# Kernel optimization log

Measured on AMD Instinct MI355X. Metric: run time of the kernel, lower is better.

## Reference

```python
import jax, jax.numpy as jnp
import numpy as np

EPS = 1e-5
GN_GROUPS_DIV = 4  # nn.GroupNorm(out_ch // 4, out_ch)


def conv1x1(x, w, b=None):
    # x [B,C,H,W], w [O,C]
    y = jnp.einsum('bchw,oc->bohw', x, w)
    return y if b is None else y + b[None, :, None, None]


def conv2d(x, w, pad):
    return jax.lax.conv_general_dilated(
        x, w, (1, 1), [(pad, pad), (pad, pad)],
        dimension_numbers=('NCHW', 'OIHW', 'NCHW'))


def batchnorm(x, gamma, beta):
    # training-mode BatchNorm2d: batch statistics over (B,H,W)
    mu = jnp.mean(x, axis=(0, 2, 3), keepdims=True)
    var = jnp.var(x, axis=(0, 2, 3), keepdims=True)
    xn = (x - mu) * jax.lax.rsqrt(var + EPS)
    return xn * gamma[None, :, None, None] + beta[None, :, None, None]


def groupnorm(x, gamma, beta, groups):
    B, C, H, W = x.shape
    xg = x.reshape(B, groups, C // groups, H, W)
    mu = jnp.mean(xg, axis=(2, 3, 4), keepdims=True)
    var = jnp.var(xg, axis=(2, 3, 4), keepdims=True)
    xn = ((xg - mu) * jax.lax.rsqrt(var + EPS)).reshape(B, C, H, W)
    return xn * gamma[None, :, None, None] + beta[None, :, None, None]


def bilinear_sample(img, ys, xs):
    # Faithful to DSC._bilinear_interpolate_3D: floor/floor+1 coords are
    # clamped BEFORE computing weights, so samples exactly at the last
    # row/col get all-zero weights (output zeroed there), as in torch.
    H, W = img.shape[2], img.shape[3]
    y0 = jnp.floor(ys)
    x0 = jnp.floor(xs)
    y0c = jnp.clip(y0, 0, H - 1).astype(jnp.int32)
    y1c = jnp.clip(y0 + 1, 0, H - 1).astype(jnp.int32)
    x0c = jnp.clip(x0, 0, W - 1).astype(jnp.int32)
    x1c = jnp.clip(x0 + 1, 0, W - 1).astype(jnp.int32)
    y0f, y1f = y0c.astype(ys.dtype), y1c.astype(ys.dtype)
    x0f, x1f = x0c.astype(xs.dtype), x1c.astype(xs.dtype)
    w00 = (y1f - ys) * (x1f - xs)
    w01 = (y1f - ys) * (xs - x0f)
    w10 = (ys - y0f) * (x1f - xs)
    w11 = (ys - y0f) * (xs - x0f)
    g = lambda yy, xx: img[:, :, yy, xx]  # irregular gather, [B,C,H,W]
    return (g(y0c, x0c) * w00 + g(y0c, x1c) * w01 +
            g(y1c, x0c) * w10 + g(y1c, x1c) * w11)


def _forward(x, ca_w1, ca_w2, sa_w, gate_w, off_w, off_b, off_gamma, off_beta,
             dsc_w, dsc_b, gn_gamma, gn_beta, bn_gamma, bn_beta, prelu_a,
             out_w, out_b):
    B, C, H, W = x.shape
    res = x

    # --- ChannelAttention2D (CBAM): shared MLP on avg & max pooled desc ---
    avg = jnp.mean(x, axis=(2, 3), keepdims=True)          # [B,C,1,1]
    mx = jnp.max(x, axis=(2, 3), keepdims=True)
    mlp = lambda v: conv1x1(jax.nn.relu(conv1x1(v, ca_w1)), ca_w2)
    ca = jax.nn.sigmoid(mlp(avg) + mlp(mx))
    x_ca = x * ca

    # --- SpatialAttention2D (CBAM): 7x7 conv over [mean,max] channel maps ---
    s_avg = jnp.mean(x, axis=1, keepdims=True)
    s_max = jnp.max(x, axis=1, keepdims=True)
    sa = jax.nn.sigmoid(conv2d(jnp.concatenate([s_avg, s_max], axis=1), sa_w, pad=3))
    x_sa = x * sa

    # --- gate fuse ---
    fuse = x_sa + x_ca
    guide = jax.nn.sigmoid(conv1x1(fuse, gate_w))
    xg = x * guide

    # --- DSConv(kernel_size=1, morph=0, if_offset=True) ---
    # offset branch (computed as in torch; with num_points=1 the iterative
    # offset accumulation zeroes the center point, so offsets do NOT move
    # the sampling grid -> zero gradient flows to the offset conv)
    off = jnp.tanh(batchnorm(conv2d(xg, off_w, pad=1) + off_b[None, :, None, None],
                             off_gamma, off_beta))
    del off  # dead in fwd math for kernel_size=1 (faithful to source)

    ii = jnp.arange(H, dtype=x.dtype)[:, None] * jnp.ones((1, W), x.dtype)
    jj = jnp.ones((H, 1), x.dtype) * jnp.arange(W, dtype=x.dtype)[None, :]
    deformed = bilinear_sample(xg, ii, jj)  # identity gather except last row/col zeroed

    d = conv1x1(deformed, dsc_w, dsc_b)     # dsc_conv_x with (k,1)=(1,1) kernel
    d = groupnorm(d, gn_gamma, gn_beta, C // GN_GROUPS_DIV)
    d = jax.nn.relu(d)

    # --- residual + BN + PReLU + 1x1 out conv ---
    y = d + res
    y = batchnorm(y, bn_gamma, bn_beta)
    a = prelu_a.reshape(())
    y = jnp.where(y >= 0, y, a * y)
    return conv1x1(y, out_w, out_b)         # [B,1,H,W]


def setup_inputs() -> dict:
    key = jax.random.key(0)
    ks = jax.random.split(key, 12)
    B, C, H, W = 8, 64, 256, 256
    r = C // 16  # CBAM ratio 16
    f32 = jnp.float32
    n = lambda k, shp, s: (jax.random.normal(k, shp, dtype=f32) * s)
    return {
        'x': n(ks[0], (B, C, H, W), 1.0),
        'ca_w1': n(ks[1], (r, C), 0.1),
        'ca_w2': n(ks[2], (C, r), 0.1),
        'sa_w': n(ks[3], (1, 2, 7, 7), 0.1),
        'gate_w': n(ks[4], (C, C), 0.05),
        'off_w': n(ks[5], (2, C, 3, 3), 0.05),
        'off_b': jnp.zeros((2,), f32),
        'off_gamma': jnp.ones((2,), f32),
        'off_beta': jnp.zeros((2,), f32),
        'dsc_w': n(ks[6], (C, C), 0.05),
        'dsc_b': jnp.zeros((C,), f32),
        'gn_gamma': jnp.ones((C,), f32),
        'gn_beta': jnp.zeros((C,), f32),
        'bn_gamma': jnp.ones((C,), f32),
        'bn_beta': jnp.zeros((C,), f32),
        'prelu_a': jnp.full((1,), 0.25, f32),
        'out_w': n(ks[7], (1, C), 0.1),
        'out_b': jnp.zeros((1,), f32),
    }


def reference(x, ca_w1, ca_w2, sa_w, gate_w, off_w, off_b, off_gamma, off_beta,
              dsc_w, dsc_b, gn_gamma, gn_beta, bn_gamma, bn_beta, prelu_a,
              out_w, out_b):
    return _forward(x, ca_w1, ca_w2, sa_w, gate_w, off_w, off_b, off_gamma,
                    off_beta, dsc_w, dsc_b, gn_gamma, gn_beta, bn_gamma,
                    bn_beta, prelu_a, out_w, out_b)
```

## Files before the change

### kernel.cpp

```cpp
#include <hip/hip_runtime.h>

#define HW 65536
#define CB 64
#define NB 8

typedef __attribute__((ext_vector_type(4))) float f32x4;
typedef __attribute__((ext_vector_type(8))) short s16x8;

__device__ __forceinline__ float sigm(float v) { return 1.f / (1.f + __expf(-v)); }

__device__ __forceinline__ unsigned encf(float f) {
    unsigned u = __float_as_uint(f);
    return (u & 0x80000000u) ? ~u : (u | 0x80000000u);
}
__device__ __forceinline__ float decf(unsigned u) {
    return (u & 0x80000000u) ? __uint_as_float(u & 0x7fffffffu) : __uint_as_float(~u);
}
__device__ __forceinline__ unsigned f2bf(float f) {
    unsigned u = __float_as_uint(f);
    u += 0x7fffu + ((u >> 16) & 1u);
    return u >> 16;
}
__device__ __forceinline__ float bf2f(unsigned h) {
    return __uint_as_float(h << 16);
}
__device__ __forceinline__ int swz(int row, int w) { return (row << 5) + (w ^ ((row & 7) << 2)); }

__global__ __launch_bounds__(256) void k_init(
    const float* __restrict__ gw, const float* __restrict__ dw,
    unsigned* __restrict__ wbuf, unsigned* __restrict__ stats)
{
    const int t = threadIdx.x;
    if (blockIdx.x < 2) {
        const float* src = (blockIdx.x == 0) ? gw : dw;
        unsigned* dst = wbuf + (blockIdx.x << 11);
        const int orow = t >> 2, cq = (t & 3) << 4;
        const float* s = src + (orow << 6) + cq;
        unsigned u[8];
        #pragma unroll
        for (int j = 0; j < 8; ++j)
            u[j] = f2bf(s[2 * j]) | (f2bf(s[2 * j + 1]) << 16);
        const int wbase = (t & 3) << 3;
        *(uint4*)&dst[swz(orow, wbase)]     = make_uint4(u[0], u[1], u[2], u[3]);
        *(uint4*)&dst[swz(orow, wbase + 4)] = make_uint4(u[4], u[5], u[6], u[7]);
    } else {
        const int base = (blockIdx.x - 2) * 4736;
        #pragma unroll
        for (int k = 0; k < 19; ++k) {
            const int idx = base + k * 256 + t;
            if (idx < base + 4736 && idx < 9472) stats[idx] = 0u;
        }
    }
}

__global__ __launch_bounds__(256) void k_pre(
    const float* __restrict__ x, unsigned short* __restrict__ xpc,
    float* __restrict__ pool_scr, unsigned* __restrict__ pmax_scr,
    unsigned* __restrict__ sm)
{
    __shared__ unsigned tile[8192];
    __shared__ float scrS[8][64];
    __shared__ float scrM[8][64];
    const int t = threadIdx.x;
    const int b = blockIdx.x >> 8;
    const int pbase = (blockIdx.x & 255) << 8;
    const size_t xb = ((size_t)(b << 6)) * HW + pbase + t;
    const int s = (t & 7) << 2;

    float psum = 0.f, pmax = -1e30f;
    #pragma unroll
    for (int cg = 0; cg < 4; ++cg) {
        float v[16];
        #pragma unroll
        for (int k = 0; k < 16; ++k)
            v[k] = x[xb + (size_t)((cg << 4) + k) * HW];
        #pragma unroll
        for (int k = 0; k < 16; ++k) { psum += v[k]; pmax = fmaxf(pmax, v[k]); }
        unsigned w[8];
        #pragma unroll
        for (int k = 0; k < 8; ++k) w[k] = f2bf(v[2 * k]) | (f2bf(v[2 * k + 1]) << 16);
        *(uint4*)&tile[(t << 5) + (((cg << 3)) ^ s)]     = make_uint4(w[0], w[1], w[2], w[3]);
        *(uint4*)&tile[(t << 5) + (((cg << 3) + 4) ^ s)] = make_uint4(w[4], w[5], w[6], w[7]);
    }
    sm[(size_t)b * HW + pbase + t] = f2bf(psum * (1.f / 64.f)) | (f2bf(pmax) << 16);
    __syncthreads();

    {
        const int cp = t & 31, q = t >> 5;
        float s0 = 0.f, s1 = 0.f, m0 = -1e30f, m1 = -1e30f;
        #pragma unroll 8
        for (int i = 0; i < 32; ++i) {
            const int px = (q << 5) + i;
            const unsigned u = tile[(px << 5) + (cp ^ ((px & 7) << 2))];
            const float a0 = bf2f(u & 0xffffu), a1 = bf2f(u >> 16);
            s0 += a0; s1 += a1;
            m0 = fmaxf(m0, a0); m1 = fmaxf(m1, a1);
        }
        scrS[q][2 * cp] = s0; scrS[q][2 * cp + 1] = s1;
        scrM[q][2 * cp] = m0; scrM[q][2 * cp + 1] = m1;
    }
    {
        unsigned short* xp = xpc + (((size_t)b * HW + pbase) << 6);
        #pragma unroll
        for (int k = 0; k < 8; ++k) {
            const int px = (k << 5) + (t >> 3);
            const int w = ((t & 7) << 2) ^ ((px & 7) << 2);
            const uint4 v = *(const uint4*)&tile[(px << 5) + w];
            *(uint4*)(xp + (k << 11) + (t << 3)) = v;
        }
    }
    __syncthreads();
    if (t < 64) {
        float ss = 0.f, mm = -1e30f;
        #pragma unroll
        for (int q = 0; q < 8; ++q) { ss += scrS[q][t]; mm = fmaxf(mm, scrM[q][t]); }
        const int copy = blockIdx.x & 7;
        atomicAdd(&pool_scr[(((b << 3) + copy) << 6) + t], ss);
        atomicMax(&pmax_scr[(((b << 3) + copy) << 6) + t], encf(mm));
    }
}

__global__ __launch_bounds__(256) void k_sa_ca(
    const unsigned* __restrict__ sm, const float* __restrict__ w,
    const float* __restrict__ pool_scr, const unsigned* __restrict__ pmax_scr,
    const float* __restrict__ w1, const float* __restrict__ w2,
    unsigned short* __restrict__ sa, float* __restrict__ ca)
{
    const int t = threadIdx.x;
    const int b = blockIdx.x >> 8;
    const int pix = ((blockIdx.x & 255) << 8) | t;
    const int i = pix >> 8, j = pix & 255;
    const unsigned* src = sm + (size_t)b * HW;
    float acc = 0.f;
    #pragma unroll
    for (int ki = 0; ki < 7; ++ki) {
        const int y = i + ki - 3;
        if ((unsigned)y < 256u) {
            #pragma unroll
            for (int kj = 0; kj < 7; ++kj) {
                const int xx = j + kj - 3;
                if ((unsigned)xx < 256u) {
                    const unsigned u = src[(y << 8) | xx];
                    acc += bf2f(u & 0xffffu) * w[ki * 7 + kj] +
                           bf2f(u >> 16)     * w[49 + ki * 7 + kj];
                }
            }
        }
    }
    sa[(size_t)b * HW + pix] = (unsigned short)f2bf(sigm(acc));

    if ((blockIdx.x & 255) == 0) {
        __shared__ float av[CB], mv[CB], hh[8];
        if (t < CB) {
            float ss = 0.f; unsigned mm = 0u;
            #pragma unroll
            for (int r = 0; r < 8; ++r) {
                ss += pool_scr[(((b << 3) + r) << 6) + t];
                mm = max(mm, pmax_scr[(((b << 3) + r) << 6) + t]);
            }
            av[t] = ss * (1.f / (float)HW);
            mv[t] = decf(mm);
        }
        __syncthreads();
        if (t < 8) {
            const int h = t & 3;
            const float* v = (t < 4) ? av : mv;
            float ssum = 0;
            for (int c = 0; c < CB; ++c) ssum += w1[h * CB + c] * v[c];
            hh[t] = fmaxf(ssum, 0.f);
        }
        __syncthreads();
        if (t < CB) {
            float ssum = 0;
            #pragma unroll
            for (int h = 0; h < 4; ++h) ssum += w2[t * 4 + h] * (hh[h] + hh[4 + h]);
            ca[b * CB + t] = sigm(ssum);
        }
    }
}

__global__ __launch_bounds__(256, 3) void k_main(
    const unsigned short* __restrict__ xpc, const unsigned short* __restrict__ sa,
    const float* __restrict__ ca, const unsigned* __restrict__ wbuf,
    const float* __restrict__ db,
    unsigned short* __restrict__ dbuf, float* __restrict__ gn_sum,
    float* __restrict__ gn_sq)
{
    __shared__ unsigned lds[12320];
    __shared__ float saL[128];
    __shared__ float caL[64];
    const int t = threadIdx.x;
    const int wv = t >> 6, l = t & 63, hi = l >> 4, lo = l & 15;
    const int b = blockIdx.x >> 9;
    const int pbase = (blockIdx.x & 511) << 7;

    #pragma unroll
    for (int k = 0; k < 4; ++k) {
        const int idx = (k << 8) + t;
        *(uint4*)&lds[idx << 2] = *(const uint4*)&wbuf[idx << 2];
    }
    if (t < 128) saL[t] = bf2f(sa[(size_t)b * HW + pbase + t]);
    else if (t < 192) caL[t - 128] = ca[(b << 6) + (t - 128)];

    {
        const unsigned short* xp = xpc + (((size_t)b * HW + pbase) << 6);
        #pragma unroll
        for (int k = 0; k < 4; ++k) {
            const int idx = (k << 8) + t;
            const int px = idx >> 3;
            const int wg = (idx & 7) << 2;
            const uint4 v = *(const uint4*)(xp + (idx << 3));
            *(uint4*)&lds[8192 + (px << 5) + (wg ^ ((px & 7) << 2))] = v;
        }
    }
    __syncthreads();

    {
        const int wb2 = (wv << 3) + (hi << 1);
        const int cbb = wb2 << 1;
        const float c0 = caL[cbb], c1 = caL[cbb + 1], c2 = caL[cbb + 2], c3 = caL[cbb + 3];
        #pragma unroll
        for (int n = 0; n < 8; ++n) {
            const int pxl = (n << 4) + lo;
            const float sv = saL[pxl];
            const uint2 xv = *(const uint2*)&lds[8192 + swz(pxl, wb2)];
            uint2 o;
            o.x = f2bf(bf2f(xv.x & 0xffffu) * (sv + c0)) | (f2bf(bf2f(xv.x >> 16) * (sv + c1)) << 16);
            o.y = f2bf(bf2f(xv.y & 0xffffu) * (sv + c2)) | (f2bf(bf2f(xv.y >> 16) * (sv + c3)) << 16);
            *(uint2*)&lds[4096 + swz(pxl, wb2)] = o;
        }
    }
    __syncthreads();

    f32x4 acc[8];
    #pragma unroll
    for (int n = 0; n < 8; ++n) acc[n] = (f32x4){0.f, 0.f, 0.f, 0.f};
    {
        const int arow = (wv << 4) + lo;
        const s16x8 a0 = __builtin_bit_cast(s16x8, *(const uint4*)&lds[swz(arow, hi << 2)]);
        const s16x8 a1 = __builtin_bit_cast(s16x8, *(const uint4*)&lds[swz(arow, (hi << 2) + 16)]);
        #pragma unroll
        for (int n = 0; n < 8; ++n) {
            const int brow = (n << 4) + lo;
            const s16x8 b0 = __builtin_bit_cast(s16x8, *(const uint4*)&lds[4096 + swz(brow, hi << 2)]);
            const s16x8 b1 = __builtin_bit_cast(s16x8, *(const uint4*)&lds[4096 + swz(brow, (hi << 2) + 16)]);
            acc[n] = __builtin_amdgcn_mfma_f32_16x16x32_bf16(a0, b0, acc[n], 0, 0, 0);
            acc[n] = __builtin_amdgcn_mfma_f32_16x16x32_bf16(a1, b1, acc[n], 0, 0, 0);
        }
    }
    __syncthreads();

    {
        const bool row255 = (pbase >> 8) == 255;
        const bool halfblk = (pbase & 128) != 0;
        const int wb2 = (wv << 3) + (hi << 1);
        #pragma unroll
        for (int n = 0; n < 8; ++n) {
            const int pxl = (n << 4) + lo;
            const uint2 xv = *(const uint2*)&lds[8192 + swz(pxl, wb2)];
            const bool zero = row255 || (halfblk && pxl == 127);
            float xg0 = zero ? 0.f : bf2f(xv.x & 0xffffu) * sigm(acc[n][0]);
            float xg1 = zero ? 0.f : bf2f(xv.x >> 16)     * sigm(acc[n][1]);
            float xg2 = zero ? 0.f : bf2f(xv.y & 0xffffu) * sigm(acc[n][2]);
            float xg3 = zero ? 0.f : bf2f(xv.y >> 16)     * sigm(acc[n][3]);
            uint2 o;
            o.x = f2bf(xg0) | (f2bf(xg1) << 16);
            o.y = f2bf(xg2) | (f2bf(xg3) << 16);
            *(uint2*)&lds[4096 + swz(pxl, wb2)] = o;
        }
    }
    __syncthreads();

    f32x4 acc2[8];
    #pragma unroll
    for (int n = 0; n < 8; ++n) acc2[n] = (f32x4){0.f, 0.f, 0.f, 0.f};
    {
        const int arow = (wv << 4) + lo;
        const s16x8 a0 = __builtin_bit_cast(s16x8, *(const uint4*)&lds[2048 + swz(arow, hi << 2)]);
        const s16x8 a1 = __builtin_bit_cast(s16x8, *(const uint4*)&lds[2048 + swz(arow, (hi << 2) + 16)]);
        #pragma unroll
        for (int n = 0; n < 8; ++n) {
            const int brow = (n << 4) + lo;
            const s16x8 b0 = __builtin_bit_cast(s16x8, *(const uint4*)&lds[4096 + swz(brow, hi << 2)]);
            const s16x8 b1 = __builtin_bit_cast(s16x8, *(const uint4*)&lds[4096 + swz(brow, (hi << 2) + 16)]);
            acc2[n] = __builtin_amdgcn_mfma_f32_16x16x32_bf16(a0, b0, acc2[n], 0, 0, 0);
            acc2[n] = __builtin_amdgcn_mfma_f32_16x16x32_bf16(a1, b1, acc2[n], 0, 0, 0);
        }
    }

    float gs = 0.f, gq = 0.f;
    {
        const float4 bv = *(const float4*)(db + (wv << 4) + (hi << 2));
        unsigned short* dp = dbuf + (((size_t)b * HW + pbase) << 6) + (wv << 4) + (hi << 2);
        #pragma unroll
        for (int n = 0; n < 8; ++n) {
            const int pxl = (n << 4) + lo;
            const float d0 = acc2[n][0] + bv.x, d1 = acc2[n][1] + bv.y;
            const float d2 = acc2[n][2] + bv.z, d3 = acc2[n][3] + bv.w;
            gs += d0 + d1 + d2 + d3;
            gq += d0 * d0 + d1 * d1 + d2 * d2 + d3 * d3;
            uint2 o;
            o.x = f2bf(d0) | (f2bf(d1) << 16);
            o.y = f2bf(d2) | (f2bf(d3) << 16);
            *(uint2*)(dp + ((size_t)pxl << 6)) = o;
        }
    }
    #pragma unroll
    for (int o = 1; o < 16; o <<= 1) { gs += __shfl_xor(gs, o); gq += __shfl_xor(gq, o); }
    float* smf = (float*)&lds[12288];
    if (lo == 0) { smf[(((wv << 2) + hi) << 1)] = gs; smf[(((wv << 2) + hi) << 1) + 1] = gq; }
    __syncthreads();
    if (t < 16) {
        atomicAdd(&gn_sum[(b << 4) + t], smf[2 * t]);
        atomicAdd(&gn_sq[(b << 4) + t],  smf[2 * t + 1]);
    }
}

__global__ __launch_bounds__(256) void k_gnbn(
    const unsigned short* __restrict__ xpc, unsigned short* __restrict__ dy,
    const float* __restrict__ gn_sum, const float* __restrict__ gn_sq,
    const float* __restrict__ gamma, const float* __restrict__ beta,
    float* __restrict__ bn_scr)
{
    const int t = threadIdx.x;
    const size_t P0 = (size_t)blockIdx.x << 8;
    const int b = (int)(P0 >> 16);
    __shared__ float ga[CB], gb[CB];
    __shared__ float red[4][128];
    if (t < CB) {
        const int g = t >> 2;
        const float n4 = 4.f * (float)HW;
        const float mu = gn_sum[b * 16 + g] / n4;
        const float var = gn_sq[b * 16 + g] / n4 - mu * mu;
        const float a = rsqrtf(var + 1e-5f) * gamma[t];
        ga[t] = a; gb[t] = beta[t] - mu * a;
    }
    __syncthreads();
    const int o8 = (t & 7) << 3;
    float ar[8], br[8];
    #pragma unroll
    for (int k = 0; k < 8; ++k) { ar[k] = ga[o8 + k]; br[k] = gb[o8 + k]; }
    float as[8], aq[8];
    #pragma unroll
    for (int k = 0; k < 8; ++k) { as[k] = 0.f; aq[k] = 0.f; }
    for (int i = 0; i < 8; ++i) {
        const size_t P = P0 + (i << 5) + (t >> 3);
        const size_t idx = (P << 6) + o8;
        const uint4 dv = *(const uint4*)(dy + idx);
        const uint4 xv = *(const uint4*)(xpc + idx);
        const unsigned dw_[4] = {dv.x, dv.y, dv.z, dv.w};
        const unsigned xw_[4] = {xv.x, xv.y, xv.z, xv.w};
        uint4 o;
        unsigned ow_[4];
        #pragma unroll
        for (int p = 0; p < 4; ++p) {
            const int k0 = 2 * p;
            const float y0 = fmaxf(bf2f(dw_[p] & 0xffffu) * ar[k0] + br[k0], 0.f) + bf2f(xw_[p] & 0xffffu);
            const float y1 = fmaxf(bf2f(dw_[p] >> 16) * ar[k0 + 1] + br[k0 + 1], 0.f) + bf2f(xw_[p] >> 16);
            as[k0] += y0; aq[k0] += y0 * y0;
            as[k0 + 1] += y1; aq[k0 + 1] += y1 * y1;
            ow_[p] = f2bf(y0) | (f2bf(y1) << 16);
        }
        o.x = ow_[0]; o.y = ow_[1]; o.z = ow_[2]; o.w = ow_[3];
        *(uint4*)(dy + idx) = o;
    }
    #pragma unroll
    for (int k = 0; k < 8; ++k) {
        #pragma unroll
        for (int m = 8; m < 64; m <<= 1) {
            as[k] += __shfl_xor(as[k], m);
            aq[k] += __shfl_xor(aq[k], m);
        }
    }
    if ((t & 63) < 8) {
        const int o = t & 7, wvv = t >> 6;
        #pragma unroll
        for (int k = 0; k < 8; ++k) {
            red[wvv][o * 16 + k] = as[k];
            red[wvv][o * 16 + 8 + k] = aq[k];
        }
    }
    __syncthreads();
    if (t < 128) {
        const int o = t >> 4, st = (t >> 3) & 1, k = t & 7;
        const float v = red[0][t] + red[1][t] + red[2][t] + red[3][t];
        atomicAdd(&bn_scr[(blockIdx.x & 7) * 128 + st * 64 + o * 8 + k], v);
    }
}

__global__ __launch_bounds__(256) void k_out(
    const unsigned short* __restrict__ y, const float* __restrict__ bn_scr,
    const float* __restrict__ gamma, const float* __restrict__ beta,
    const float* __restrict__ pa, const float* __restrict__ ow,
    const float* __restrict__ ob, float* __restrict__ out)
{
    const int t = threadIdx.x;
    __shared__ float A[CB], Bs[CB], W[CB];
    if (t < CB) {
        float s = 0.f, q = 0.f;
        #pragma unroll
        for (int r = 0; r < 8; ++r) { s += bn_scr[r * 128 + t]; q += bn_scr[r * 128 + 64 + t]; }
        const float n = (float)NB * (float)HW;
        const float mu = s / n;
        const float var = q / n - mu * mu;
        const float a = rsqrtf(var + 1e-5f) * gamma[t];
        A[t] = a; Bs[t] = beta[t] - mu * a; W[t] = ow[t];
    }
    __syncthreads();
    const size_t P = ((size_t)blockIdx.x << 8) + t;
    const unsigned short* yp = y + (P << 6);
    const float alpha = pa[0];
    float acc = ob[0];
    #pragma unroll
    for (int q = 0; q < 8; ++q) {
        const uint4 v = *(const uint4*)(yp + (q << 3));
        const unsigned vw[4] = {v.x, v.y, v.z, v.w};
        #pragma unroll
        for (int p = 0; p < 4; ++p) {
            const int c = (q << 3) + 2 * p;
            float z0 = bf2f(vw[p] & 0xffffu) * A[c] + Bs[c];
            float z1 = bf2f(vw[p] >> 16) * A[c + 1] + Bs[c + 1];
            z0 = z0 >= 0.f ? z0 : alpha * z0;
            z1 = z1 >= 0.f ? z1 : alpha * z1;
            acc += W[c] * z0 + W[c + 1] * z1;
        }
    }
    out[P] = acc;
}

extern "C" void kernel_launch(void* const* d_in, const int* in_sizes, int n_in,
                              void* d_out, int out_size, void* d_ws, size_t ws_size,
                              hipStream_t stream)
{
    const float* x        = (const float*)d_in[0];
    const float* ca_w1    = (const float*)d_in[1];
    const float* ca_w2    = (const float*)d_in[2];
    const float* sa_w     = (const float*)d_in[3];
    const float* gate_w   = (const float*)d_in[4];
    const float* dsc_w    = (const float*)d_in[9];
    const float* dsc_b    = (const float*)d_in[10];
    const float* gn_gamma = (const float*)d_in[11];
    const float* gn_beta  = (const float*)d_in[12];
    const float* bn_gamma = (const float*)d_in[13];
    const float* bn_beta  = (const float*)d_in[14];
    const float* prelu_a  = (const float*)d_in[15];
    const float* out_w    = (const float*)d_in[16];
    const float* out_b    = (const float*)d_in[17];
    float* out = (float*)d_out;

    char* ws = (char*)d_ws;
    size_t off = 0;
    auto alloc = [&](size_t bytes) -> char* {
        char* p = ws + off;
        off = (off + bytes + 255) & ~(size_t)255;
        return p;
    };
    unsigned short* dbuf = (unsigned short*)alloc((size_t)NB * HW * CB * 2);
    unsigned short* xpc  = (unsigned short*)alloc((size_t)NB * HW * CB * 2);
    unsigned* smb        = (unsigned*)alloc((size_t)NB * HW * 4);
    unsigned short* sab  = (unsigned short*)alloc((size_t)NB * HW * 2);
    unsigned* wbuf       = (unsigned*)alloc(4096 * 4);
    float* cav   = (float*)alloc(512 * 4);
    char* stats  = alloc(9472 * 4);
    float*    pool_scr = (float*)stats;
    unsigned* pmax_scr = (unsigned*)(stats + 4096 * 4);
    float*    gn_sum   = (float*)(stats + 8192 * 4);
    float*    gn_sq    = (float*)(stats + 8320 * 4);
    float*    bn_scr   = (float*)(stats + 8448 * 4);
    (void)in_sizes; (void)n_in; (void)out_size; (void)ws_size;

    k_init <<<4,        256, 0, stream>>>(gate_w, dsc_w, wbuf, (unsigned*)stats);
    k_pre  <<<NB * 256, 256, 0, stream>>>(x, xpc, pool_scr, pmax_scr, smb);
    k_sa_ca<<<NB * 256, 256, 0, stream>>>(smb, sa_w, pool_scr, pmax_scr,
                                          ca_w1, ca_w2, sab, cav);
    k_main <<<NB * 512, 256, 0, stream>>>(xpc, sab, cav, wbuf, dsc_b,
                                          dbuf, gn_sum, gn_sq);
    k_gnbn <<<2048,     256, 0, stream>>>(xpc, dbuf, gn_sum, gn_sq, gn_gamma, gn_beta, bn_scr);
    k_out  <<<2048,     256, 0, stream>>>(dbuf, bn_scr, bn_gamma, bn_beta,
                                          prelu_a, out_w, out_b, out);
}
```

Baseline: 164.6 us.

## Fold init into k_pre, drop pooling atomics, load weights to registers in k_main

Removes the separate k_init launch by adding three extra blocks to k_pre that convert the weights and zero the stats. Channel pooling partials are now written per block without atomics and reduced over 256 entries in k_sa_ca. In k_main the gate and dsc weight fragments are read straight from global memory into registers, and the attention scaling is fused into the LDS fill stage. This shrinks LDS use so occupancy can be raised to 4 blocks. The costs are a serial 256-step reduction in one block per batch and register pressure at the higher occupancy.

```diff
diff --git a/kernel.cpp b/kernel.cpp
--- a/kernel.cpp
+++ b/kernel.cpp
@@ -9,13 +9,6 @@
 
 __device__ __forceinline__ float sigm(float v) { return 1.f / (1.f + __expf(-v)); }
 
-__device__ __forceinline__ unsigned encf(float f) {
-    unsigned u = __float_as_uint(f);
-    return (u & 0x80000000u) ? ~u : (u | 0x80000000u);
-}
-__device__ __forceinline__ float decf(unsigned u) {
-    return (u & 0x80000000u) ? __uint_as_float(u & 0x7fffffffu) : __uint_as_float(~u);
-}
 __device__ __forceinline__ unsigned f2bf(float f) {
     unsigned u = __float_as_uint(f);
     u += 0x7fffu + ((u >> 16) & 1u);
@@ -26,42 +19,38 @@
 }
 __device__ __forceinline__ int swz(int row, int w) { return (row << 5) + (w ^ ((row & 7) << 2)); }
 
-__global__ __launch_bounds__(256) void k_init(
-    const float* __restrict__ gw, const float* __restrict__ dw,
-    unsigned* __restrict__ wbuf, unsigned* __restrict__ stats)
-{
-    const int t = threadIdx.x;
-    if (blockIdx.x < 2) {
-        const float* src = (blockIdx.x == 0) ? gw : dw;
-        unsigned* dst = wbuf + (blockIdx.x << 11);
-        const int orow = t >> 2, cq = (t & 3) << 4;
-        const float* s = src + (orow << 6) + cq;
-        unsigned u[8];
-        #pragma unroll
-        for (int j = 0; j < 8; ++j)
-            u[j] = f2bf(s[2 * j]) | (f2bf(s[2 * j + 1]) << 16);
-        const int wbase = (t & 3) << 3;
-        *(uint4*)&dst[swz(orow, wbase)]     = make_uint4(u[0], u[1], u[2], u[3]);
-        *(uint4*)&dst[swz(orow, wbase + 4)] = make_uint4(u[4], u[5], u[6], u[7]);
-    } else {
-        const int base = (blockIdx.x - 2) * 4736;
-        #pragma unroll
-        for (int k = 0; k < 19; ++k) {
-            const int idx = base + k * 256 + t;
-            if (idx < base + 4736 && idx < 9472) stats[idx] = 0u;
-        }
-    }
-}
-
 __global__ __launch_bounds__(256) void k_pre(
     const float* __restrict__ x, unsigned short* __restrict__ xpc,
-    float* __restrict__ pool_scr, unsigned* __restrict__ pmax_scr,
-    unsigned* __restrict__ sm)
-{
+    float* __restrict__ pool_scr, float* __restrict__ pmax_scr,
+    unsigned* __restrict__ sm,
+    const float* __restrict__ gw, const float* __restrict__ dw,
+    unsigned* __restrict__ wbuf, float* __restrict__ zstats)
+{
+    const int t = threadIdx.x;
+    if (blockIdx.x >= NB * 256) {
+        const int ex = blockIdx.x - NB * 256;
+        if (ex < 2) {
+            const float* src = (ex == 0) ? gw : dw;
+            unsigned* dst = wbuf + (ex << 11);
+            const int orow = t >> 2, cq = (t & 3) << 4;
+            const float* s = src + (orow << 6) + cq;
+            unsigned u[8];
+            #pragma unroll
+            for (int j = 0; j < 8; ++j)
+                u[j] = f2bf(s[2 * j]) | (f2bf(s[2 * j + 1]) << 16);
+            const int wbase = (t & 3) << 3;
+            *(uint4*)&dst[swz(orow, wbase)]     = make_uint4(u[0], u[1], u[2], u[3]);
+            *(uint4*)&dst[swz(orow, wbase + 4)] = make_uint4(u[4], u[5], u[6], u[7]);
+        } else {
+            #pragma unroll
+            for (int k2 = 0; k2 < 5; ++k2) zstats[k2 * 256 + t] = 0.f;
+        }
+        return;
+    }
+
     __shared__ unsigned tile[8192];
     __shared__ float scrS[8][64];
     __shared__ float scrM[8][64];
-    const int t = threadIdx.x;
     const int b = blockIdx.x >> 8;
     const int pbase = (blockIdx.x & 255) << 8;
     const size_t xb = ((size_t)(b << 6)) * HW + pbase + t;
@@ -114,15 +103,14 @@
         float ss = 0.f, mm = -1e30f;
         #pragma unroll
         for (int q = 0; q < 8; ++q) { ss += scrS[q][t]; mm = fmaxf(mm, scrM[q][t]); }
-        const int copy = blockIdx.x & 7;
-        atomicAdd(&pool_scr[(((b << 3) + copy) << 6) + t], ss);
-        atomicMax(&pmax_scr[(((b << 3) + copy) << 6) + t], encf(mm));
+        pool_scr[((size_t)blockIdx.x << 6) + t] = ss;
+        pmax_scr[((size_t)blockIdx.x << 6) + t] = mm;
     }
 }
 
 __global__ __launch_bounds__(256) void k_sa_ca(
     const unsigned* __restrict__ sm, const float* __restrict__ w,
-    const float* __restrict__ pool_scr, const unsigned* __restrict__ pmax_scr,
+    const float* __restrict__ pool_scr, const float* __restrict__ pmax_scr,
     const float* __restrict__ w1, const float* __restrict__ w2,
     unsigned short* __restrict__ sa, float* __restrict__ ca)
 {
@@ -152,14 +140,13 @@
     if ((blockIdx.x & 255) == 0) {
         __shared__ float av[CB], mv[CB], hh[8];
         if (t < CB) {
-            float ss = 0.f; unsigned mm = 0u;
-            #pragma unroll
-            for (int r = 0; r < 8; ++r) {
-                ss += pool_scr[(((b << 3) + r) << 6) + t];
-                mm = max(mm, pmax_scr[(((b << 3) + r) << 6) + t]);
+            float ss = 0.f, mm = -1e30f;
+            for (int r = 0; r < 256; ++r) {
+                ss += pool_scr[(((size_t)(b << 8) + r) << 6) + t];
+                mm = fmaxf(mm, pmax_scr[(((size_t)(b << 8) + r) << 6) + t]);
             }
             av[t] = ss * (1.f / (float)HW);
-            mv[t] = decf(mm);
+            mv[t] = mm;
         }
         __syncthreads();
         if (t < 8) {
@@ -179,28 +166,24 @@
     }
 }
 
-__global__ __launch_bounds__(256, 3) void k_main(
+__global__ __launch_bounds__(256, 4) void k_main(
     const unsigned short* __restrict__ xpc, const unsigned short* __restrict__ sa,
     const float* __restrict__ ca, const unsigned* __restrict__ wbuf,
     const float* __restrict__ db,
     unsigned short* __restrict__ dbuf, float* __restrict__ gn_sum,
     float* __restrict__ gn_sq)
 {
-    __shared__ unsigned lds[12320];
-    __shared__ float saL[128];
-    __shared__ float caL[64];
+    __shared__ unsigned lds[8224];
     const int t = threadIdx.x;
     const int wv = t >> 6, l = t & 63, hi = l >> 4, lo = l & 15;
     const int b = blockIdx.x >> 9;
     const int pbase = (blockIdx.x & 511) << 7;
 
-    #pragma unroll
-    for (int k = 0; k < 4; ++k) {
-        const int idx = (k << 8) + t;
-        *(uint4*)&lds[idx << 2] = *(const uint4*)&wbuf[idx << 2];
-    }
-    if (t < 128) saL[t] = bf2f(sa[(size_t)b * HW + pbase + t]);
-    else if (t < 192) caL[t - 128] = ca[(b << 6) + (t - 128)];
+    const int arow = (wv << 4) + lo;
+    const s16x8 ag0 = __builtin_bit_cast(s16x8, *(const uint4*)&wbuf[swz(arow, hi << 2)]);
+    const s16x8 ag1 = __builtin_bit_cast(s16x8, *(const uint4*)&wbuf[swz(arow, (hi << 2) + 16)]);
+    const s16x8 ad0 = __builtin_bit_cast(s16x8, *(const uint4*)&wbuf[2048 + swz(arow, hi << 2)]);
+    const s16x8 ad1 = __builtin_bit_cast(s16x8, *(const uint4*)&wbuf[2048 + swz(arow, (hi << 2) + 16)]);
 
     {
         const unsigned short* xp = xpc + (((size_t)b * HW + pbase) << 6);
@@ -208,26 +191,24 @@
         for (int k = 0; k < 4; ++k) {
             const int idx = (k << 8) + t;
             const int px = idx >> 3;
+            const int ch0 = (idx & 7) << 3;
             const int wg = (idx & 7) << 2;
             const uint4 v = *(const uint4*)(xp + (idx << 3));
-            *(uint4*)&lds[8192 + (px << 5) + (wg ^ ((px & 7) << 2))] = v;
-        }
-    }
-    __syncthreads();
-
-    {
-        const int wb2 = (wv << 3) + (hi << 1);
-        const int cbb = wb2 << 1;
-        const float c0 = caL[cbb], c1 = caL[cbb + 1], c2 = caL[cbb + 2], c3 = caL[cbb + 3];
-        #pragma unroll
-        for (int n = 0; n < 8; ++n) {
-            const int pxl = (n << 4) + lo;
-            const float sv = saL[pxl];
-            const uint2 xv = *(const uint2*)&lds[8192 + swz(pxl, wb2)];
-            uint2 o;
-            o.x = f2bf(bf2f(xv.x & 0xffffu) * (sv + c0)) | (f2bf(bf2f(xv.x >> 16) * (sv + c1)) << 16);
-            o.y = f2bf(bf2f(xv.y & 0xffffu) * (sv + c2)) | (f2bf(bf2f(xv.y >> 16) * (sv + c3)) << 16);
-            *(uint2*)&lds[4096 + swz(pxl, wb2)] = o;
+            const float sv = bf2f(sa[(size_t)b * HW + pbase + px]);
+            const float4 cv0 = *(const float4*)(ca + (b << 6) + ch0);
+            const float4 cv1 = *(const float4*)(ca + (b << 6) + ch0 + 4);
+            uint4 fv;
+            fv.x = f2bf(bf2f(v.x & 0xffffu) * (sv + cv0.x)) |
+                   (f2bf(bf2f(v.x >> 16)    * (sv + cv0.y)) << 16);
+            fv.y = f2bf(bf2f(v.y & 0xffffu) * (sv + cv0.z)) |
+                   (f2bf(bf2f(v.y >> 16)    * (sv + cv0.w)) << 16);
+            fv.z = f2bf(bf2f(v.z & 0xffffu) * (sv + cv1.x)) |
+                   (f2bf(bf2f(v.z >> 16)    * (sv + cv1.y)) << 16);
+            fv.w = f2bf(bf2f(v.w & 0xffffu) * (sv + cv1.z)) |
+                   (f2bf(bf2f(v.w >> 16)    * (sv + cv1.w)) << 16);
+            const int off = (px << 5) + (wg ^ ((px & 7) << 2));
+            *(uint4*)&lds[4096 + off] = v;
+            *(uint4*)&lds[off]        = fv;
         }
     }
     __syncthreads();
@@ -235,18 +216,13 @@
     f32x4 acc[8];
     #pragma unroll
     for (int n = 0; n < 8; ++n) acc[n] = (f32x4){0.f, 0.f, 0.f, 0.f};
-    {
-        const int arow = (wv << 4) + lo;
-        const s16x8 a0 = __builtin_bit_cast(s16x8, *(const uint4*)&lds[swz(arow, hi << 2)]);
-        const s16x8 a1 = __builtin_bit_cast(s16x8, *(const uint4*)&lds[swz(arow, (hi << 2) + 16)]);
-        #pragma unroll
-        for (int n = 0; n < 8; ++n) {
-            const int brow = (n << 4) + lo;
-            const s16x8 b0 = __builtin_bit_cast(s16x8, *(const uint4*)&lds[4096 + swz(brow, hi << 2)]);
-            const s16x8 b1 = __builtin_bit_cast(s16x8, *(const uint4*)&lds[4096 + swz(brow, (hi << 2) + 16)]);
-            acc[n] = __builtin_amdgcn_mfma_f32_16x16x32_bf16(a0, b0, acc[n], 0, 0, 0);
-            acc[n] = __builtin_amdgcn_mfma_f32_16x16x32_bf16(a1, b1, acc[n], 0, 0, 0);
-        }
+    #pragma unroll
+    for (int n = 0; n < 8; ++n) {
+        const int brow = (n << 4) + lo;
+        const s16x8 b0 = __builtin_bit_cast(s16x8, *(const uint4*)&lds[swz(brow, hi << 2)]);
+        const s16x8 b1 = __builtin_bit_cast(s16x8, *(const uint4*)&lds[swz(brow, (hi << 2) + 16)]);
+        acc[n] = __builtin_amdgcn_mfma_f32_16x16x32_bf16(ag0, b0, acc[n], 0, 0, 0);
+        acc[n] = __builtin_amdgcn_mfma_f32_16x16x32_bf16(ag1, b1, acc[n], 0, 0, 0);
     }
     __syncthreads();
 
@@ -257,7 +233,7 @@
         #pragma unroll
         for (int n = 0; n < 8; ++n) {
             const int pxl = (n << 4) + lo;
-            const uint2 xv = *(const uint2*)&lds[8192 + swz(pxl, wb2)];
+            const uint2 xv = *(const uint2*)&lds[4096 + swz(pxl, wb2)];
             const bool zero = row255 || (halfblk && pxl == 127);
             float xg0 = zero ? 0.f : bf2f(xv.x & 0xffffu) * sigm(acc[n][0]);
             float xg1 = zero ? 0.f : bf2f(xv.x >> 16)     * sigm(acc[n][1]);
@@ -266,7 +242,7 @@
             uint2 o;
             o.x = f2bf(xg0) | (f2bf(xg1) << 16);
             o.y = f2bf(xg2) | (f2bf(xg3) << 16);
-            *(uint2*)&lds[4096 + swz(pxl, wb2)] = o;
+            *(uint2*)&lds[swz(pxl, wb2)] = o;
         }
     }
     __syncthreads();
@@ -274,18 +250,13 @@
     f32x4 acc2[8];
     #pragma unroll
     for (int n = 0; n < 8; ++n) acc2[n] = (f32x4){0.f, 0.f, 0.f, 0.f};
-    {
-        const int arow = (wv << 4) + lo;
-        const s16x8 a0 = __builtin_bit_cast(s16x8, *(const uint4*)&lds[2048 + swz(arow, hi << 2)]);
-        const s16x8 a1 = __builtin_bit_cast(s16x8, *(const uint4*)&lds[2048 + swz(arow, (hi << 2) + 16)]);
-        #pragma unroll
-        for (int n = 0; n < 8; ++n) {
-            const int brow = (n << 4) + lo;
-            const s16x8 b0 = __builtin_bit_cast(s16x8, *(const uint4*)&lds[4096 + swz(brow, hi << 2)]);
-            const s16x8 b1 = __builtin_bit_cast(s16x8, *(const uint4*)&lds[4096 + swz(brow, (hi << 2) + 16)]);
-            acc2[n] = __builtin_amdgcn_mfma_f32_16x16x32_bf16(a0, b0, acc2[n], 0, 0, 0);
-            acc2[n] = __builtin_amdgcn_mfma_f32_16x16x32_bf16(a1, b1, acc2[n], 0, 0, 0);
-        }
+    #pragma unroll
+    for (int n = 0; n < 8; ++n) {
+        const int brow = (n << 4) + lo;
+        const s16x8 b0 = __builtin_bit_cast(s16x8, *(const uint4*)&lds[swz(brow, hi << 2)]);
+        const s16x8 b1 = __builtin_bit_cast(s16x8, *(const uint4*)&lds[swz(brow, (hi << 2) + 16)]);
+        acc2[n] = __builtin_amdgcn_mfma_f32_16x16x32_bf16(ad0, b0, acc2[n], 0, 0, 0);
+        acc2[n] = __builtin_amdgcn_mfma_f32_16x16x32_bf16(ad1, b1, acc2[n], 0, 0, 0);
     }
 
     float gs = 0.f, gq = 0.f;
@@ -307,7 +278,7 @@
     }
     #pragma unroll
     for (int o = 1; o < 16; o <<= 1) { gs += __shfl_xor(gs, o); gq += __shfl_xor(gq, o); }
-    float* smf = (float*)&lds[12288];
+    float* smf = (float*)&lds[8192];
     if (lo == 0) { smf[(((wv << 2) + hi) << 1)] = gs; smf[(((wv << 2) + hi) << 1) + 1] = gq; }
     __syncthreads();
     if (t < 16) {
@@ -460,22 +431,23 @@
     unsigned* smb        = (unsigned*)alloc((size_t)NB * HW * 4);
     unsigned short* sab  = (unsigned short*)alloc((size_t)NB * HW * 2);
     unsigned* wbuf       = (unsigned*)alloc(4096 * 4);
-    float* cav   = (float*)alloc(512 * 4);
-    char* stats  = alloc(9472 * 4);
-    float*    pool_scr = (float*)stats;
-    unsigned* pmax_scr = (unsigned*)(stats + 4096 * 4);
-    float*    gn_sum   = (float*)(stats + 8192 * 4);
-    float*    gn_sq    = (float*)(stats + 8320 * 4);
-    float*    bn_scr   = (float*)(stats + 8448 * 4);
+    float* cav           = (float*)alloc(512 * 4);
+    float* pool_scr      = (float*)alloc(2048 * 64 * 4);
+    float* pmax_scr      = (float*)alloc(2048 * 64 * 4);
+    float* zstats        = (float*)alloc(1280 * 4);
+    float* gn_sum = zstats;
+    float* gn_sq  = zstats + 128;
+    float* bn_scr = zstats + 256;
     (void)in_sizes; (void)n_in; (void)out_size; (void)ws_size;
 
-    k_init <<<4,        256, 0, stream>>>(gate_w, dsc_w, wbuf, (unsigned*)stats);
-    k_pre  <<<NB * 256, 256, 0, stream>>>(x, xpc, pool_scr, pmax_scr, smb);
-    k_sa_ca<<<NB * 256, 256, 0, stream>>>(smb, sa_w, pool_scr, pmax_scr,
-                                          ca_w1, ca_w2, sab, cav);
-    k_main <<<NB * 512, 256, 0, stream>>>(xpc, sab, cav, wbuf, dsc_b,
-                                          dbuf, gn_sum, gn_sq);
-    k_gnbn <<<2048,     256, 0, stream>>>(xpc, dbuf, gn_sum, gn_sq, gn_gamma, gn_beta, bn_scr);
-    k_out  <<<2048,     256, 0, stream>>>(dbuf, bn_scr, bn_gamma, bn_beta,
-                                          prelu_a, out_w, out_b, out);
-}
+    k_pre  <<<NB * 256 + 3, 256, 0, stream>>>(x, xpc, pool_scr, pmax_scr, smb,
+                                              gate_w, dsc_w, wbuf, zstats);
+    k_sa_ca<<<NB * 256,     256, 0, stream>>>(smb, sa_w, pool_scr, pmax_scr,
+                                              ca_w1, ca_w2, sab, cav);
+    k_main <<<NB * 512,     256, 0, stream>>>(xpc, sab, cav, wbuf, dsc_b,
+                                              dbuf, gn_sum, gn_sq);
+    k_gnbn <<<2048,         256, 0, stream>>>(xpc, dbuf, gn_sum, gn_sq,
+                                              gn_gamma, gn_beta, bn_scr);
+    k_out  <<<2048,         256, 0, stream>>>(dbuf, bn_scr, bn_gamma, bn_beta,
+                                              prelu_a, out_w, out_b, out);
+}
```

New measurement: 159.7 us, median of 2. 1.03x faster.
